# Kernel tuning notes

Hardware: AMD Instinct MI355X
Metric: run time of the kernel (lower is better)

The kernel has to match this reference:

```python
import jax, jax.numpy as jnp
import numpy as np

B, L, D, H = 4, 2048, 1024, 16
DV = D // H


def setup_inputs() -> dict:
    key = jax.random.key(0)
    ks = jax.random.split(key, 11)
    s = 1.0 / np.sqrt(D)
    return {
        "query": jax.random.normal(ks[0], (B, L, D), jnp.float32),
        "key": jax.random.normal(ks[1], (B, L, D), jnp.float32),
        "value": jax.random.normal(ks[2], (B, L, D), jnp.float32),
        "Wq": jax.random.normal(ks[3], (D, D), jnp.float32) * s,
        "bq": jnp.zeros((D,), jnp.float32),
        "Wk": jax.random.normal(ks[4], (D, D), jnp.float32) * s,
        "bk": jnp.zeros((D,), jnp.float32),
        "Wv": jax.random.normal(ks[5], (D, D), jnp.float32) * s,
        "bv": jnp.zeros((D,), jnp.float32),
        "Wc": jax.random.normal(ks[6], (D, D), jnp.float32) * s,
        "bc": jnp.zeros((D,), jnp.float32),
    }


def _split(x):
    # [B, L, D] -> [B, H, L, DV]
    b, l, d = x.shape
    return x.reshape(b, l, H, DV).transpose(0, 2, 1, 3)


def reference(query, key, value, Wq, bq, Wk, bk, Wv, bv, Wc, bc):
    # Linear projections (torch Linear: x @ W.T + b)
    hq = _split(query @ Wq.T + bq)
    hk = _split(key @ Wk.T + bk)
    hv = _split(value @ Wv.T + bv)
    scale = 1.0 / jnp.sqrt(jnp.float32(DV))
    scores = jnp.einsum("bhqd,bhkd->bhqk", hq, hk) * scale  # [B,H,L,L]
    p = jax.nn.softmax(scores, axis=-1)
    out = jnp.einsum("bhqk,bhkd->bhqd", p, hv)  # [B,H,L,DV]
    out = out.transpose(0, 2, 1, 3).reshape(out.shape[0], out.shape[2], D)
    return out @ Wc.T + bc
```

## Files before the change

### kernel.cpp

```cpp
#include <hip/hip_runtime.h>

#define DI __device__ __forceinline__

typedef __attribute__((ext_vector_type(8))) short bf16x8;
typedef __attribute__((ext_vector_type(4))) float f32x4;
typedef __attribute__((ext_vector_type(16))) float f32x16;
typedef __attribute__((ext_vector_type(4))) unsigned u32x4;
typedef __attribute__((ext_vector_type(2))) unsigned u32x2;

static constexpr int B_ = 4, L_ = 2048, D_ = 1024, H_ = 16, DV_ = 64;
static constexpr int M_ = B_ * L_;
static constexpr float SCALE_LOG2 = 0.18033688011112042f;

DI short f2b(float f) {
  union { float f; unsigned u; } v; v.f = f;
  unsigned r = v.u + 0x7FFFu + ((v.u >> 16) & 1u);
  return (short)(r >> 16);
}

DI float b2f(short s) {
  union { unsigned u; float f; } v;
  v.u = ((unsigned)(unsigned short)s) << 16;
  return v.f;
}

DI unsigned cvtpk(float lo, float hi) {
  unsigned r;
  asm("v_cvt_pk_bf16_f32 %0, %1, %2" : "=v"(r) : "v"(lo), "v"(hi));
  return r;
}

DI void gl_lds16(const void* g, void* l) {
  __builtin_amdgcn_global_load_lds(
      (const __attribute__((address_space(1))) unsigned int*)g,
      (__attribute__((address_space(3))) unsigned int*)l, 16, 0, 0);
}

#define MFMA16(a, b, c) __builtin_amdgcn_mfma_f32_16x16x32_bf16((a), (b), (c), 0, 0, 0)
#define MFMA32(a, b, c) __builtin_amdgcn_mfma_f32_32x32x16_bf16((a), (b), (c), 0, 0, 0)

__global__ __launch_bounds__(256) void cvtw_kernel(const float* __restrict__ W0,
                                                   const float* __restrict__ W1,
                                                   const float* __restrict__ W2,
                                                   const float* __restrict__ W3,
                                                   short* __restrict__ dst) {
  const int p = blockIdx.y;
  const float* s = p == 0 ? W0 : p == 1 ? W1 : p == 2 ? W2 : W3;
  short* d = dst + (size_t)p * 1048576;
  int i0 = (blockIdx.x * 256 + threadIdx.x) * 8;
  int stride = gridDim.x * 256 * 8;
  for (int i = i0; i < 1048576; i += stride) {
    float4 a = *(const float4*)(s + i);
    float4 b = *(const float4*)(s + i + 4);
    u32x4 o;
    o[0] = cvtpk(a.x, a.y);
    o[1] = cvtpk(a.z, a.w);
    o[2] = cvtpk(b.x, b.y);
    o[3] = cvtpk(b.z, b.w);
    *(u32x4*)(d + i) = o;
  }
}

__global__ __launch_bounds__(256) void gemm_qkvf(const float* __restrict__ Xq,
                                                 const float* __restrict__ Xk,
                                                 const float* __restrict__ Xv,
                                                 const short* __restrict__ Wall,
                                                 const float* __restrict__ bq,
                                                 const float* __restrict__ bk,
                                                 const float* __restrict__ bv,
                                                 short* __restrict__ Hq,
                                                 short* __restrict__ Hk,
                                                 short* __restrict__ Hv) {
  constexpr int K = 1024, N = 1024;
  __shared__ float Asf[128 * 32];
  __shared__ short Bs[128 * 32];
  const int p = blockIdx.y;
  const float* A = p == 0 ? Xq : p == 1 ? Xk : Xv;
  const short* Wt = Wall + (size_t)p * 1048576;
  const float* bias = p == 0 ? bq : p == 1 ? bk : bv;
  short* outb = p == 0 ? Hq : p == 1 ? Hk : Hv;

  const int tid = threadIdx.x;
  const int w = tid >> 6, lane = tid & 63;
  const int c = lane & 15, g = lane >> 4;
  const int bid = (blockIdx.x & 7) * 64 + (blockIdx.x >> 3);
  const int bn = bid & 7, bm = bid >> 3;
  const int wr = w >> 1, wc = w & 1;

  f32x4 acc[4][4] = {};

  for (int kt = 0; kt < K / 32; ++kt) {
    __syncthreads();
#pragma unroll
    for (int it = 0; it < 4; ++it) {
      int slot = it * 256 + tid;
      int row = slot >> 3, ch = (slot & 7) ^ (row & 7);
      gl_lds16(A + ((size_t)(bm * 128 + row) * K + kt * 32 + ch * 4),
               &Asf[(it * 256 + w * 64) * 4]);
    }
#pragma unroll
    for (int ia = 0; ia < 2; ++ia) {
      int slot = ia * 256 + tid;
      int row = slot >> 2, ch = slot & 3;
      gl_lds16(Wt + ((size_t)(bn * 128 + row) * K + kt * 32 + ch * 8),
               &Bs[(ia * 256 + w * 64) * 8]);
    }
    __syncthreads();
    bf16x8 af[4], bf[4];
#pragma unroll
    for (int mi = 0; mi < 4; ++mi) {
      int r = wr * 64 + mi * 16 + c;
      int c0 = (((2 * g) ^ (r & 7)) * 4);
      int c1 = (((2 * g + 1) ^ (r & 7)) * 4);
      float4 lo = *(const float4*)&Asf[r * 32 + c0];
      float4 hi = *(const float4*)&Asf[r * 32 + c1];
      u32x4 pk;
      pk[0] = cvtpk(lo.x, lo.y);
      pk[1] = cvtpk(lo.z, lo.w);
      pk[2] = cvtpk(hi.x, hi.y);
      pk[3] = cvtpk(hi.z, hi.w);
      af[mi] = __builtin_bit_cast(bf16x8, pk);
    }
#pragma unroll
    for (int ni = 0; ni < 4; ++ni)
      bf[ni] = *(const bf16x8*)&Bs[(wc * 64 + ni * 16 + c) * 32 + g * 8];
#pragma unroll
    for (int mi = 0; mi < 4; ++mi)
#pragma unroll
      for (int ni = 0; ni < 4; ++ni)
        acc[mi][ni] = MFMA16(af[mi], bf[ni], acc[mi][ni]);
  }

  float bvv[4];
#pragma unroll
  for (int ni = 0; ni < 4; ++ni) bvv[ni] = bias[bn * 128 + wc * 64 + ni * 16 + c];
#pragma unroll
  for (int mi = 0; mi < 4; ++mi)
#pragma unroll
    for (int ni = 0; ni < 4; ++ni)
#pragma unroll
      for (int j = 0; j < 4; ++j) {
        int row = bm * 128 + wr * 64 + mi * 16 + g * 4 + j;
        int col = bn * 128 + wc * 64 + ni * 16 + c;
        outb[(size_t)row * N + col] = f2b(acc[mi][ni][j] + bvv[ni]);
      }
}

template <int OUTF32>
__global__ __launch_bounds__(256) void gemm_bt(const short* __restrict__ A,
                                               const short* __restrict__ Wt,
                                               const float* __restrict__ bias,
                                               float* __restrict__ outf,
                                               short* __restrict__ outb) {
  constexpr int K = 1024, N = 1024;
  __shared__ short As[128 * 32];
  __shared__ short Bs[128 * 32];
  const int tid = threadIdx.x;
  const int w = tid >> 6, lane = tid & 63;
  const int c = lane & 15, g = lane >> 4;
  const int bid = (blockIdx.x & 7) * 64 + (blockIdx.x >> 3);
  const int bn = bid & 7, bm = bid >> 3;
  const int wr = w >> 1, wc = w & 1;

  f32x4 acc[4][4] = {};

  for (int kt = 0; kt < K / 32; ++kt) {
    __syncthreads();
#pragma unroll
    for (int ia = 0; ia < 2; ++ia) {
      int slot = ia * 256 + tid;
      int row = slot >> 2, ch = slot & 3;
      gl_lds16(A + ((size_t)(bm * 128 + row) * K + kt * 32 + ch * 8),
               &As[(ia * 256 + w * 64) * 8]);
      gl_lds16(Wt + ((size_t)(bn * 128 + row) * K + kt * 32 + ch * 8),
               &Bs[(ia * 256 + w * 64) * 8]);
    }
    __syncthreads();
    bf16x8 af[4], bf[4];
#pragma unroll
    for (int mi = 0; mi < 4; ++mi)
      af[mi] = *(const bf16x8*)&As[(wr * 64 + mi * 16 + c) * 32 + g * 8];
#pragma unroll
    for (int ni = 0; ni < 4; ++ni)
      bf[ni] = *(const bf16x8*)&Bs[(wc * 64 + ni * 16 + c) * 32 + g * 8];
#pragma unroll
    for (int mi = 0; mi < 4; ++mi)
#pragma unroll
      for (int ni = 0; ni < 4; ++ni)
        acc[mi][ni] = MFMA16(af[mi], bf[ni], acc[mi][ni]);
  }

  float bv[4];
#pragma unroll
  for (int ni = 0; ni < 4; ++ni) bv[ni] = bias[bn * 128 + wc * 64 + ni * 16 + c];
#pragma unroll
  for (int mi = 0; mi < 4; ++mi)
#pragma unroll
    for (int ni = 0; ni < 4; ++ni)
#pragma unroll
      for (int j = 0; j < 4; ++j) {
        int row = bm * 128 + wr * 64 + mi * 16 + g * 4 + j;
        int col = bn * 128 + wc * 64 + ni * 16 + c;
        float v = acc[mi][ni][j] + bv[ni];
        if (OUTF32)
          outf[(size_t)row * N + col] = v;
        else
          outb[(size_t)row * N + col] = f2b(v);
      }
}

__global__ __launch_bounds__(256) void transpose_kernel(const short* __restrict__ Hv,
                                                        short* __restrict__ Hvt) {
  __shared__ short T[64 * 72];
  int bid = blockIdx.x;
  const int lt = bid & 31;
  const int h = (bid >> 5) & 15;
  const int b = bid >> 9;
  const int l0 = lt * 64;
  const int tid = threadIdx.x;
#pragma unroll
  for (int it = 0; it < 2; ++it) {
    int slot = it * 256 + tid;
    int r = slot >> 3, ch = slot & 7;
    bf16x8 v = *(const bf16x8*)&Hv[(size_t)(b * L_ + l0 + r) * D_ + h * DV_ + ch * 8];
    *(bf16x8*)&T[r * 72 + ch * 8] = v;
  }
  __syncthreads();
#pragma unroll
  for (int it = 0; it < 2; ++it) {
    int slot = it * 256 + tid;
    int dv = slot >> 3, ch = slot & 7;
    bf16x8 o;
#pragma unroll
    for (int i = 0; i < 8; ++i) o[i] = T[(ch * 8 + i) * 72 + dv];
    *(bf16x8*)&Hvt[(size_t)((b * H_ + h) * DV_ + dv) * L_ + l0 + ch * 8] = o;
  }
}

__global__ __launch_bounds__(512, 2) void attn_kernel(const short* __restrict__ Hq,
                                                      const short* __restrict__ Hk,
                                                      const short* __restrict__ Hvt,
                                                      short* __restrict__ Aout) {
  __shared__ __align__(16) short lds[33280];
  const int tid = threadIdx.x;
  const int w = tid >> 6, lane = tid & 63;
  const int c31 = lane & 31, g1 = lane >> 5;
  const int sw = (blockIdx.x & 7) * 64 + (blockIdx.x >> 3);
  const int qb = sw & 7;
  const int h = (sw >> 3) & 15;
  const int b = sw >> 7;
  const int q0 = qb * 256;

  const short* qptr = Hq + (size_t)(b * L_ + q0 + w * 32 + c31) * D_ + h * 64 + g1 * 8;
  bf16x8 qf[4];
#pragma unroll
  for (int ks = 0; ks < 4; ++ks) {
    bf16x8 raw = *(const bf16x8*)(qptr + ks * 16);
    u32x4 pk;
#pragma unroll
    for (int i = 0; i < 4; ++i)
      pk[i] = cvtpk(b2f(raw[2 * i]) * SCALE_LOG2, b2f(raw[2 * i + 1]) * SCALE_LOG2);
    qf[ks] = __builtin_bit_cast(bf16x8, pk);
  }

  f32x16 O0 = {}, O1 = {};
  float ls = 0.f;
  unsigned* Pw = (unsigned*)(lds + 16384) + w * 1056;

  auto stage = [&](int buf, int kv0) {
    short* Kb = lds + buf * 8192;
    short* Vb = Kb + 4096;
    int row = tid >> 3;
    int ch = (tid & 7) ^ (row & 7);
    gl_lds16(Hk + (size_t)(b * L_ + kv0 + row) * D_ + h * 64 + ch * 8, Kb + w * 512);
    gl_lds16(Hvt + (size_t)((b * H_ + h) * DV_ + row) * L_ + kv0 + ch * 8, Vb + w * 512);
  };

  stage(0, 0);
  int cur = 0;
  for (int t = 0; t < L_ / 64; ++t) {
    __syncthreads();
    if (t + 1 < L_ / 64) stage(cur ^ 1, (t + 1) * 64);
    const short* Kb = lds + cur * 8192;
    const short* Vb = Kb + 4096;

    f32x16 s0 = {}, s1 = {};
    __builtin_amdgcn_s_setprio(1);
#pragma unroll
    for (int ks = 0; ks < 4; ++ks) {
      int cp = (((2 * ks + g1) ^ (c31 & 7)) * 8);
      bf16x8 k0 = *(const bf16x8*)(Kb + c31 * 64 + cp);
      bf16x8 k1 = *(const bf16x8*)(Kb + (32 + c31) * 64 + cp);
      s0 = MFMA32(k0, qf[ks], s0);
      s1 = MFMA32(k1, qf[ks], s1);
    }
    __builtin_amdgcn_s_setprio(0);

    float rs = 0.f;
#pragma unroll
    for (int i = 0; i < 8; ++i) {
      float a0 = __builtin_amdgcn_exp2f(s0[2 * i]);
      float a1 = __builtin_amdgcn_exp2f(s0[2 * i + 1]);
      float c0 = __builtin_amdgcn_exp2f(s1[2 * i]);
      float c1 = __builtin_amdgcn_exp2f(s1[2 * i + 1]);
      rs += (a0 + a1) + (c0 + c1);
      int kr = (i & 1) + 4 * (i >> 1) + 2 * g1;
      Pw[kr * 33 + c31] = cvtpk(a0, a1);
      Pw[(16 + kr) * 33 + c31] = cvtpk(c0, c1);
    }
    ls += rs + __shfl_xor(rs, 32);

    __builtin_amdgcn_s_setprio(1);
#pragma unroll
    for (int ks2 = 0; ks2 < 4; ++ks2) {
      const unsigned* pb = Pw + (ks2 * 8 + g1 * 4) * 33 + c31;
      u32x4 pk;
      pk[0] = pb[0];
      pk[1] = pb[33];
      pk[2] = pb[66];
      pk[3] = pb[99];
      bf16x8 pf = __builtin_bit_cast(bf16x8, pk);
      int cp = (((2 * ks2 + g1) ^ (c31 & 7)) * 8);
      bf16x8 vf0 = *(const bf16x8*)(Vb + c31 * 64 + cp);
      bf16x8 vf1 = *(const bf16x8*)(Vb + (32 + c31) * 64 + cp);
      O0 = MFMA32(vf0, pf, O0);
      O1 = MFMA32(vf1, pf, O1);
    }
    __builtin_amdgcn_s_setprio(0);
    cur ^= 1;
  }

  float inv = 1.0f / ls;
  __syncthreads();
  short* Os = lds;
#pragma unroll
  for (int dt = 0; dt < 2; ++dt) {
#pragma unroll
    for (int rq = 0; rq < 4; ++rq) {
      float e0 = (dt ? O1[4 * rq] : O0[4 * rq]) * inv;
      float e1 = (dt ? O1[4 * rq + 1] : O0[4 * rq + 1]) * inv;
      float e2 = (dt ? O1[4 * rq + 2] : O0[4 * rq + 2]) * inv;
      float e3 = (dt ? O1[4 * rq + 3] : O0[4 * rq + 3]) * inv;
      u32x2 pr;
      pr[0] = cvtpk(e0, e1);
      pr[1] = cvtpk(e2, e3);
      int q = w * 32 + c31;
      int dv = dt * 32 + 8 * rq + 4 * g1;
      *(u32x2*)&Os[q * 72 + dv] = pr;
    }
  }
  __syncthreads();
  const int r = tid >> 1, hf = tid & 1;
  const size_t obase = (size_t)(b * L_ + q0 + r) * D_ + h * 64 + hf * 32;
#pragma unroll
  for (int cc = 0; cc < 4; ++cc) {
    bf16x8 vv = *(const bf16x8*)&Os[r * 72 + hf * 32 + cc * 8];
    *(bf16x8*)&Aout[obase + cc * 8] = vv;
  }
}

extern "C" void kernel_launch(void* const* d_in, const int* in_sizes, int n_in,
                              void* d_out, int out_size, void* d_ws, size_t ws_size,
                              hipStream_t stream) {
  (void)in_sizes; (void)n_in; (void)out_size; (void)ws_size;
  const float* q = (const float*)d_in[0];
  const float* k = (const float*)d_in[1];
  const float* v = (const float*)d_in[2];
  const float* Wq = (const float*)d_in[3];
  const float* bq = (const float*)d_in[4];
  const float* Wk = (const float*)d_in[5];
  const float* bk = (const float*)d_in[6];
  const float* Wv = (const float*)d_in[7];
  const float* bv = (const float*)d_in[8];
  const float* Wc = (const float*)d_in[9];
  const float* bc = (const float*)d_in[10];
  float* out = (float*)d_out;

  short* ws = (short*)d_ws;
  const size_t SZ = (size_t)M_ * D_;
  const size_t WSZ = (size_t)D_ * D_;
  short* wqb = ws;
  short* wcb = ws + 3 * WSZ;
  short* hq = ws + 4 * WSZ;
  short* hk = hq + SZ;
  short* hv = hk + SZ;
  short* hvt = hv + SZ;
  short* aout = hv;

  dim3 gw(128, 4);
  cvtw_kernel<<<gw, 256, 0, stream>>>(Wq, Wk, Wv, Wc, wqb);

  dim3 gq(512, 3);
  gemm_qkvf<<<gq, 256, 0, stream>>>(q, k, v, wqb, bq, bk, bv, hq, hk, hv);

  transpose_kernel<<<2048, 256, 0, stream>>>(hv, hvt);

  attn_kernel<<<512, 512, 0, stream>>>(hq, hk, hvt, aout);

  gemm_bt<1><<<512, 256, 0, stream>>>(aout, wcb, bc, out, nullptr);
}
```

Measured before the change: 205.8 us.

## Process two 32-row query tiles per wave in attention kernel with 256 threads

The attention block drops from 8 to 4 waves, and each wave now handles 64 query rows as two 32-row tiles. Each K and V fragment read from LDS feeds twice as many MFMAs, which cuts LDS read traffic per unit of math. The cost is more accumulator registers per thread (four f32x16 outputs plus four score tiles), which raises register pressure and may limit occupancy. There are also fewer waves per block to hide latency, and staging now takes two loads per thread.

```diff
diff --git a/kernel.cpp b/kernel.cpp
--- a/kernel.cpp
+++ b/kernel.cpp
@@ -237,7 +237,7 @@
   }
 }
 
-__global__ __launch_bounds__(512, 2) void attn_kernel(const short* __restrict__ Hq,
+__global__ __launch_bounds__(256, 2) void attn_kernel(const short* __restrict__ Hq,
                                                       const short* __restrict__ Hk,
                                                       const short* __restrict__ Hvt,
                                                       short* __restrict__ Aout) {
@@ -251,29 +251,41 @@
   const int b = sw >> 7;
   const int q0 = qb * 256;
 
-  const short* qptr = Hq + (size_t)(b * L_ + q0 + w * 32 + c31) * D_ + h * 64 + g1 * 8;
-  bf16x8 qf[4];
-#pragma unroll
-  for (int ks = 0; ks < 4; ++ks) {
-    bf16x8 raw = *(const bf16x8*)(qptr + ks * 16);
-    u32x4 pk;
-#pragma unroll
-    for (int i = 0; i < 4; ++i)
-      pk[i] = cvtpk(b2f(raw[2 * i]) * SCALE_LOG2, b2f(raw[2 * i + 1]) * SCALE_LOG2);
-    qf[ks] = __builtin_bit_cast(bf16x8, pk);
-  }
-
-  f32x16 O0 = {}, O1 = {};
-  float ls = 0.f;
-  unsigned* Pw = (unsigned*)(lds + 16384) + w * 1056;
+  bf16x8 qf0[4], qf1[4];
+#pragma unroll
+  for (int hh = 0; hh < 2; ++hh) {
+    const short* qptr =
+        Hq + (size_t)(b * L_ + q0 + w * 64 + hh * 32 + c31) * D_ + h * 64 + g1 * 8;
+#pragma unroll
+    for (int ks = 0; ks < 4; ++ks) {
+      bf16x8 raw = *(const bf16x8*)(qptr + ks * 16);
+      u32x4 pk;
+#pragma unroll
+      for (int i = 0; i < 4; ++i)
+        pk[i] = cvtpk(b2f(raw[2 * i]) * SCALE_LOG2, b2f(raw[2 * i + 1]) * SCALE_LOG2);
+      if (hh == 0) qf0[ks] = __builtin_bit_cast(bf16x8, pk);
+      else         qf1[ks] = __builtin_bit_cast(bf16x8, pk);
+    }
+  }
+
+  f32x16 O00 = {}, O01 = {}, O10 = {}, O11 = {};
+  float ls0 = 0.f, ls1 = 0.f;
+  unsigned* Pw0 = (unsigned*)(lds + 16384) + (w * 2 + 0) * 1056;
+  unsigned* Pw1 = (unsigned*)(lds + 16384) + (w * 2 + 1) * 1056;
 
   auto stage = [&](int buf, int kv0) {
     short* Kb = lds + buf * 8192;
     short* Vb = Kb + 4096;
-    int row = tid >> 3;
-    int ch = (tid & 7) ^ (row & 7);
-    gl_lds16(Hk + (size_t)(b * L_ + kv0 + row) * D_ + h * 64 + ch * 8, Kb + w * 512);
-    gl_lds16(Hvt + (size_t)((b * H_ + h) * DV_ + row) * L_ + kv0 + ch * 8, Vb + w * 512);
+#pragma unroll
+    for (int it = 0; it < 2; ++it) {
+      int slot = it * 256 + tid;
+      int row = slot >> 3;
+      int ch = (slot & 7) ^ (row & 7);
+      gl_lds16(Hk + (size_t)(b * L_ + kv0 + row) * D_ + h * 64 + ch * 8,
+               Kb + (it * 256 + w * 64) * 8);
+      gl_lds16(Hvt + (size_t)((b * H_ + h) * DV_ + row) * L_ + kv0 + ch * 8,
+               Vb + (it * 256 + w * 64) * 8);
+    }
   };
 
   stage(0, 0);
@@ -284,78 +296,114 @@
     const short* Kb = lds + cur * 8192;
     const short* Vb = Kb + 4096;
 
-    f32x16 s0 = {}, s1 = {};
+    f32x16 sA0 = {}, sB0 = {}, sA1 = {}, sB1 = {};
     __builtin_amdgcn_s_setprio(1);
 #pragma unroll
     for (int ks = 0; ks < 4; ++ks) {
       int cp = (((2 * ks + g1) ^ (c31 & 7)) * 8);
       bf16x8 k0 = *(const bf16x8*)(Kb + c31 * 64 + cp);
       bf16x8 k1 = *(const bf16x8*)(Kb + (32 + c31) * 64 + cp);
-      s0 = MFMA32(k0, qf[ks], s0);
-      s1 = MFMA32(k1, qf[ks], s1);
+      sA0 = MFMA32(k0, qf0[ks], sA0);
+      sB0 = MFMA32(k1, qf0[ks], sB0);
+      sA1 = MFMA32(k0, qf1[ks], sA1);
+      sB1 = MFMA32(k1, qf1[ks], sB1);
     }
     __builtin_amdgcn_s_setprio(0);
 
-    float rs = 0.f;
-#pragma unroll
-    for (int i = 0; i < 8; ++i) {
-      float a0 = __builtin_amdgcn_exp2f(s0[2 * i]);
-      float a1 = __builtin_amdgcn_exp2f(s0[2 * i + 1]);
-      float c0 = __builtin_amdgcn_exp2f(s1[2 * i]);
-      float c1 = __builtin_amdgcn_exp2f(s1[2 * i + 1]);
-      rs += (a0 + a1) + (c0 + c1);
-      int kr = (i & 1) + 4 * (i >> 1) + 2 * g1;
-      Pw[kr * 33 + c31] = cvtpk(a0, a1);
-      Pw[(16 + kr) * 33 + c31] = cvtpk(c0, c1);
-    }
-    ls += rs + __shfl_xor(rs, 32);
+    {
+      float rs = 0.f;
+#pragma unroll
+      for (int i = 0; i < 8; ++i) {
+        float a0 = __builtin_amdgcn_exp2f(sA0[2 * i]);
+        float a1 = __builtin_amdgcn_exp2f(sA0[2 * i + 1]);
+        float c0 = __builtin_amdgcn_exp2f(sB0[2 * i]);
+        float c1 = __builtin_amdgcn_exp2f(sB0[2 * i + 1]);
+        rs += (a0 + a1) + (c0 + c1);
+        int kr = (i & 1) + 4 * (i >> 1) + 2 * g1;
+        Pw0[kr * 33 + c31] = cvtpk(a0, a1);
+        Pw0[(16 + kr) * 33 + c31] = cvtpk(c0, c1);
+      }
+      ls0 += rs + __shfl_xor(rs, 32);
+    }
+    {
+      float rs = 0.f;
+#pragma unroll
+      for (int i = 0; i < 8; ++i) {
+        float a0 = __builtin_amdgcn_exp2f(sA1[2 * i]);
+        float a1 = __builtin_amdgcn_exp2f(sA1[2 * i + 1]);
+        float c0 = __builtin_amdgcn_exp2f(sB1[2 * i]);
+        float c1 = __builtin_amdgcn_exp2f(sB1[2 * i + 1]);
+        rs += (a0 + a1) + (c0 + c1);
+        int kr = (i & 1) + 4 * (i >> 1) + 2 * g1;
+        Pw1[kr * 33 + c31] = cvtpk(a0, a1);
+        Pw1[(16 + kr) * 33 + c31] = cvtpk(c0, c1);
+      }
+      ls1 += rs + __shfl_xor(rs, 32);
+    }
 
     __builtin_amdgcn_s_setprio(1);
 #pragma unroll
     for (int ks2 = 0; ks2 < 4; ++ks2) {
-      const unsigned* pb = Pw + (ks2 * 8 + g1 * 4) * 33 + c31;
-      u32x4 pk;
-      pk[0] = pb[0];
-      pk[1] = pb[33];
-      pk[2] = pb[66];
-      pk[3] = pb[99];
-      bf16x8 pf = __builtin_bit_cast(bf16x8, pk);
       int cp = (((2 * ks2 + g1) ^ (c31 & 7)) * 8);
       bf16x8 vf0 = *(const bf16x8*)(Vb + c31 * 64 + cp);
       bf16x8 vf1 = *(const bf16x8*)(Vb + (32 + c31) * 64 + cp);
-      O0 = MFMA32(vf0, pf, O0);
-      O1 = MFMA32(vf1, pf, O1);
+      const unsigned* pb0 = Pw0 + (ks2 * 8 + g1 * 4) * 33 + c31;
+      u32x4 pk0;
+      pk0[0] = pb0[0];
+      pk0[1] = pb0[33];
+      pk0[2] = pb0[66];
+      pk0[3] = pb0[99];
+      bf16x8 pf0 = __builtin_bit_cast(bf16x8, pk0);
+      O00 = MFMA32(vf0, pf0, O00);
+      O01 = MFMA32(vf1, pf0, O01);
+      const unsigned* pb1 = Pw1 + (ks2 * 8 + g1 * 4) * 33 + c31;
+      u32x4 pk1;
+      pk1[0] = pb1[0];
+      pk1[1] = pb1[33];
+      pk1[2] = pb1[66];
+      pk1[3] = pb1[99];
+      bf16x8 pf1 = __builtin_bit_cast(bf16x8, pk1);
+      O10 = MFMA32(vf0, pf1, O10);
+      O11 = MFMA32(vf1, pf1, O11);
     }
     __builtin_amdgcn_s_setprio(0);
     cur ^= 1;
   }
 
-  float inv = 1.0f / ls;
+  float inv0 = 1.0f / ls0;
+  float inv1 = 1.0f / ls1;
   __syncthreads();
   short* Os = lds;
-#pragma unroll
-  for (int dt = 0; dt < 2; ++dt) {
-#pragma unroll
-    for (int rq = 0; rq < 4; ++rq) {
-      float e0 = (dt ? O1[4 * rq] : O0[4 * rq]) * inv;
-      float e1 = (dt ? O1[4 * rq + 1] : O0[4 * rq + 1]) * inv;
-      float e2 = (dt ? O1[4 * rq + 2] : O0[4 * rq + 2]) * inv;
-      float e3 = (dt ? O1[4 * rq + 3] : O0[4 * rq + 3]) * inv;
-      u32x2 pr;
-      pr[0] = cvtpk(e0, e1);
-      pr[1] = cvtpk(e2, e3);
-      int q = w * 32 + c31;
-      int dv = dt * 32 + 8 * rq + 4 * g1;
-      *(u32x2*)&Os[q * 72 + dv] = pr;
-    }
-  }
+#define EPI(OA, OB, INV, HH)                                        \
+  {                                                                 \
+    _Pragma("unroll") for (int dt = 0; dt < 2; ++dt) {              \
+      _Pragma("unroll") for (int rq = 0; rq < 4; ++rq) {            \
+        float e0 = (dt ? OB[4 * rq] : OA[4 * rq]) * INV;            \
+        float e1 = (dt ? OB[4 * rq + 1] : OA[4 * rq + 1]) * INV;    \
+        float e2 = (dt ? OB[4 * rq + 2] : OA[4 * rq + 2]) * INV;    \
+        float e3 = (dt ? OB[4 * rq + 3] : OA[4 * rq + 3]) * INV;    \
+        u32x2 pr;                                                   \
+        pr[0] = cvtpk(e0, e1);                                      \
+        pr[1] = cvtpk(e2, e3);                                      \
+        int q = w * 64 + (HH)*32 + c31;                             \
+        int dv = dt * 32 + 8 * rq + 4 * g1;                         \
+        *(u32x2*)&Os[q * 72 + dv] = pr;                             \
+      }                                                             \
+    }                                                               \
+  }
+  EPI(O00, O01, inv0, 0)
+  EPI(O10, O11, inv1, 1)
+#undef EPI
   __syncthreads();
-  const int r = tid >> 1, hf = tid & 1;
-  const size_t obase = (size_t)(b * L_ + q0 + r) * D_ + h * 64 + hf * 32;
-#pragma unroll
-  for (int cc = 0; cc < 4; ++cc) {
-    bf16x8 vv = *(const bf16x8*)&Os[r * 72 + hf * 32 + cc * 8];
-    *(bf16x8*)&Aout[obase + cc * 8] = vv;
+#pragma unroll
+  for (int it = 0; it < 2; ++it) {
+    const int r = it * 128 + (tid >> 1), hf = tid & 1;
+    const size_t obase = (size_t)(b * L_ + q0 + r) * D_ + h * 64 + hf * 32;
+#pragma unroll
+    for (int cc = 0; cc < 4; ++cc) {
+      bf16x8 vv = *(const bf16x8*)&Os[r * 72 + hf * 32 + cc * 8];
+      *(bf16x8*)&Aout[obase + cc * 8] = vv;
+    }
   }
 }
 
@@ -395,7 +443,7 @@
 
   transpose_kernel<<<2048, 256, 0, stream>>>(hv, hvt);
 
-  attn_kernel<<<512, 512, 0, stream>>>(hq, hk, hvt, aout);
+  attn_kernel<<<512, 256, 0, stream>>>(hq, hk, hvt, aout);
 
   gemm_bt<1><<<512, 256, 0, stream>>>(aout, wcb, bc, out, nullptr);
 }
```

New measurement: 203.7 us. No clear change (-1.0%).
